# Performance work log

Measured on AMD Instinct MI355X. Metric: run time of the kernel, lower is better.

The kernel has to match this reference:

```python
import jax, jax.numpy as jnp
import numpy as np

DIM = 1024
NUM_HEADS = 16
HEAD_DIM = DIM // NUM_HEADS
SCALE = HEAD_DIM ** -0.5


def setup_inputs() -> dict:
    key = jax.random.key(0)
    ks = jax.random.split(key, 6)
    B, N, C = 2, 2048, DIM
    std = C ** -0.5
    return {
        "x_t": jax.random.normal(ks[0], (B, N, C), dtype=jnp.float32),
        "x_s": jax.random.normal(ks[1], (B, N, C), dtype=jnp.float32),
        "W_q": jax.random.normal(ks[2], (C, C), dtype=jnp.float32) * std,
        "W_kv": jax.random.normal(ks[3], (C, 2 * C), dtype=jnp.float32) * std,
        "W_fuse": jax.random.normal(ks[4], (C, C), dtype=jnp.float32) * std,
        "b_fuse": jax.random.normal(ks[5], (C,), dtype=jnp.float32) * 0.01,
    }


def reference(x_t, x_s, W_q, W_kv, W_fuse, b_fuse):
    B, N, C = x_t.shape
    H, D = NUM_HEADS, HEAD_DIM
    # q projection (no bias, qkv_bias=False): [B,N,C] -> [B,H,N,D]
    q = (x_t @ W_q).reshape(B, N, H, D).transpose(0, 2, 1, 3)
    # kv projection: [B,N,2C] -> k,v each [B,H,N,D]
    kv = (x_s @ W_kv).reshape(B, N, 2, H, D).transpose(2, 0, 3, 1, 4)
    k, v = kv[0], kv[1]
    # attention scores [B,H,N,N]
    attn = jnp.einsum("bhnd,bhmd->bhnm", q, k) * SCALE
    attn = jax.nn.softmax(attn, axis=-1)
    # weighted values -> [B,N,C]
    a = jnp.einsum("bhnm,bhmd->bhnd", attn, v).transpose(0, 2, 1, 3).reshape(B, N, C)
    # fuse projection (with bias); dropouts are identity (p=0)
    return a @ W_fuse + b_fuse
```

## Files before the change

### kernel.cpp

```cpp
#include <hip/hip_runtime.h>

#define SEQ 2048

typedef short short8 __attribute__((ext_vector_type(8)));
typedef float floatx4 __attribute__((ext_vector_type(4)));
typedef unsigned int uint2v __attribute__((ext_vector_type(2)));
typedef unsigned int uint4v __attribute__((ext_vector_type(4)));
typedef __fp16 f16x8 __attribute__((ext_vector_type(8)));

static __device__ __forceinline__ unsigned short f2bf(float f) {
    unsigned int u = __builtin_bit_cast(unsigned int, f);
    u = (u + 0x7fffu + ((u >> 16) & 1u)) >> 16;
    return (unsigned short)u;
}

#if __has_builtin(__builtin_amdgcn_cvt_pk_bf16_f32)
typedef __bf16 bf16x2 __attribute__((ext_vector_type(2)));
static __device__ __forceinline__ unsigned int pk_bf16(float a, float b) {
    bf16x2 v = __builtin_amdgcn_cvt_pk_bf16_f32(a, b);
    return __builtin_bit_cast(unsigned int, v);
}
#else
static __device__ __forceinline__ unsigned int pk_bf16(float a, float b) {
    return (unsigned int)f2bf(a) | ((unsigned int)f2bf(b) << 16);
}
#endif

static __device__ __forceinline__ unsigned int pk_f16(float a, float b) {
    auto v = __builtin_amdgcn_cvt_pkrtz(a, b);
    return __builtin_bit_cast(unsigned int, v);
}

#define GLD16(gp, lp)                                                        \
    __builtin_amdgcn_global_load_lds(                                        \
        (const __attribute__((address_space(1))) unsigned int*)(gp),         \
        (__attribute__((address_space(3))) unsigned int*)(lp), 16, 0, 0)

__global__ void cvt2_kernel(const float4* __restrict__ a, const float4* __restrict__ b,
                            ushort4* __restrict__ oa, ushort4* __restrict__ ob, float sa) {
    int i = blockIdx.x * blockDim.x + threadIdx.x;
    if (i < 1048576) {
        float4 v = a[i];
        ushort4 o;
        o.x = f2bf(v.x * sa); o.y = f2bf(v.y * sa);
        o.z = f2bf(v.z * sa); o.w = f2bf(v.w * sa);
        oa[i] = o;
    } else {
        int j = i - 1048576;
        float4 v = b[j];
        ushort4 o;
        o.x = f2bf(v.x); o.y = f2bf(v.y);
        o.z = f2bf(v.z); o.w = f2bf(v.w);
        ob[j] = o;
    }
}

__global__ void transpose_all(const float* __restrict__ Wq, const float* __restrict__ Wkv,
                              const float* __restrict__ Wf,
                              unsigned short* __restrict__ oq, unsigned short* __restrict__ okv,
                              unsigned short* __restrict__ of_) {
    __shared__ float tile[32][33];
    int bx = blockIdx.x;
    const float* in; unsigned short* out; int N, t;
    if (bx < 1024)      { in = Wq;  out = oq;  N = 1024; t = bx; }
    else if (bx < 3072) { in = Wkv; out = okv; N = 2048; t = bx - 1024; }
    else                { in = Wf;  out = of_; N = 1024; t = bx - 3072; }
    int nb = N >> 5;
    int n0 = (t % nb) * 32, k0 = (t / nb) * 32;
    int tx = threadIdx.x, ty = threadIdx.y;
#pragma unroll
    for (int i = 0; i < 4; i++)
        tile[ty + i * 8][tx] = in[(size_t)(k0 + ty + i * 8) * N + n0 + tx];
    __syncthreads();
#pragma unroll
    for (int i = 0; i < 4; i++)
        out[(size_t)(n0 + ty + i * 8) * 1024 + k0 + tx] = f2bf(tile[tx][ty + i * 8]);
}

__global__ __launch_bounds__(256, 3)
void gemm_qkv(const unsigned short* __restrict__ xt,
              const unsigned short* __restrict__ xs,
              const unsigned short* __restrict__ wq,
              const unsigned short* __restrict__ wkv,
              unsigned short* __restrict__ q_ws,
              unsigned short* __restrict__ k_ws,
              unsigned short* __restrict__ vt_ws) {
    __shared__ unsigned short sA[128][64];
    __shared__ unsigned short sB[128][64];
    int tid = threadIdx.x, wave = tid >> 6, lane = tid & 63;
    int l15 = lane & 15, quad = lane >> 4;
    int cx = blockIdx.x;
    bool isq = cx < 8;
    const unsigned short* A  = isq ? xt : xs;
    const unsigned short* Bt = isq ? wq : wkv;
    int C0 = (isq ? cx : cx - 8) * 128;
    int R0 = blockIdx.y * 128;
    int wr = (wave >> 1) * 64, wc = (wave & 1) * 64;
    int srow = lane >> 3, scol = (lane & 7) * 8;

    floatx4 acc[4][4];
#pragma unroll
    for (int i = 0; i < 4; i++)
#pragma unroll
        for (int j = 0; j < 4; j++) acc[i][j] = (floatx4){0.f, 0.f, 0.f, 0.f};

    for (int kt = 0; kt < 16; kt++) {
        __syncthreads();
#pragma unroll
        for (int c = 0; c < 4; c++) {
            int rb = wave * 32 + c * 8;
            GLD16(&A [(size_t)(R0 + rb + srow) * 1024 + kt * 64 + scol], &sA[rb][0]);
            GLD16(&Bt[(size_t)(C0 + rb + srow) * 1024 + kt * 64 + scol], &sB[rb][0]);
        }
        __syncthreads();
#pragma unroll
        for (int ks = 0; ks < 2; ks++) {
            short8 af[4], bf[4];
#pragma unroll
            for (int mt = 0; mt < 4; mt++)
                af[mt] = *(const short8*)&sA[wr + mt * 16 + l15][ks * 32 + quad * 8];
#pragma unroll
            for (int nt = 0; nt < 4; nt++)
                bf[nt] = *(const short8*)&sB[wc + nt * 16 + l15][ks * 32 + quad * 8];
#pragma unroll
            for (int mt = 0; mt < 4; mt++)
#pragma unroll
                for (int nt = 0; nt < 4; nt++)
                    acc[mt][nt] = __builtin_amdgcn_mfma_f32_16x16x32_bf16(af[mt], bf[nt], acc[mt][nt], 0, 0, 0);
        }
    }

    int b = R0 >> 11, nb0 = (R0 & 2047) + wr;
#pragma unroll
    for (int mt = 0; mt < 4; mt++) {
#pragma unroll
        for (int nt = 0; nt < 4; nt++) {
            int col = C0 + wc + nt * 16 + l15;
            if (isq) {
                int h = col >> 6, d = col & 63;
#pragma unroll
                for (int r = 0; r < 4; r++) {
                    int n = nb0 + mt * 16 + quad * 4 + r;
                    q_ws[((size_t)((b * 16 + h) * 2048 + n)) * 64 + d] = f2bf(acc[mt][nt][r]);
                }
            } else if (col < 1024) {
                int h = col >> 6, d = col & 63;
#pragma unroll
                for (int r = 0; r < 4; r++) {
                    int n = nb0 + mt * 16 + quad * 4 + r;
                    k_ws[((size_t)((b * 16 + h) * 2048 + n)) * 64 + (d ^ ((n & 7) << 3))] = f2bf(acc[mt][nt][r]);
                }
            } else {
                int cc = col - 1024, h = cc >> 6, d = cc & 63;
                int n = nb0 + mt * 16 + quad * 4;
                uint2v pk;
                pk.x = pk_f16(acc[mt][nt][0], acc[mt][nt][1]);
                pk.y = pk_f16(acc[mt][nt][2], acc[mt][nt][3]);
                *(uint2v*)&vt_ws[((size_t)((b * 16 + h) * 64 + d)) * 2048 + n] = pk;
            }
        }
    }
}

__global__ __launch_bounds__(256, 3)
void gemm_fuse(const unsigned short* __restrict__ A,
               const unsigned short* __restrict__ Bt,
               float* __restrict__ out, const float* __restrict__ bias) {
    __shared__ unsigned short sA[128][64];
    __shared__ unsigned short sB[64][64];
    int tid = threadIdx.x, wave = tid >> 6, lane = tid & 63;
    int l15 = lane & 15, quad = lane >> 4;
    int R0 = blockIdx.y * 128, C0 = blockIdx.x * 64;
    int wr = (wave >> 1) * 64, wc = (wave & 1) * 32;
    int srow = lane >> 3, scol = (lane & 7) * 8;

    floatx4 acc[4][2];
#pragma unroll
    for (int i = 0; i < 4; i++)
#pragma unroll
        for (int j = 0; j < 2; j++) acc[i][j] = (floatx4){0.f, 0.f, 0.f, 0.f};

    for (int kt = 0; kt < 16; kt++) {
        __syncthreads();
#pragma unroll
        for (int c = 0; c < 4; c++) {
            int rb = wave * 32 + c * 8;
            GLD16(&A[(size_t)(R0 + rb + srow) * 1024 + kt * 64 + scol], &sA[rb][0]);
        }
#pragma unroll
        for (int c = 0; c < 2; c++) {
            int rb = wave * 16 + c * 8;
            GLD16(&Bt[(size_t)(C0 + rb + srow) * 1024 + kt * 64 + scol], &sB[rb][0]);
        }
        __syncthreads();
#pragma unroll
        for (int ks = 0; ks < 2; ks++) {
            short8 af[4], bf[2];
#pragma unroll
            for (int mt = 0; mt < 4; mt++)
                af[mt] = *(const short8*)&sA[wr + mt * 16 + l15][ks * 32 + quad * 8];
#pragma unroll
            for (int nt = 0; nt < 2; nt++)
                bf[nt] = *(const short8*)&sB[wc + nt * 16 + l15][ks * 32 + quad * 8];
#pragma unroll
            for (int mt = 0; mt < 4; mt++)
#pragma unroll
                for (int nt = 0; nt < 2; nt++)
                    acc[mt][nt] = __builtin_amdgcn_mfma_f32_16x16x32_bf16(af[mt], bf[nt], acc[mt][nt], 0, 0, 0);
        }
    }

#pragma unroll
    for (int mt = 0; mt < 4; mt++) {
#pragma unroll
        for (int r = 0; r < 4; r++) {
            int row = R0 + wr + mt * 16 + quad * 4 + r;
#pragma unroll
            for (int nt = 0; nt < 2; nt++) {
                int col = C0 + wc + nt * 16 + l15;
                out[(size_t)row * 1024 + col] = acc[mt][nt][r] + bias[col];
            }
        }
    }
}

__global__ __launch_bounds__(256, 2)
void attn_kernel(const unsigned short* __restrict__ Q,
                 const unsigned short* __restrict__ K,
                 const unsigned short* __restrict__ Vt,
                 unsigned short* __restrict__ Aout) {
    __shared__ __align__(16) unsigned short smem[32768];
    __shared__ float lred[4][4][16];

    int tid = threadIdx.x, wave = tid >> 6, lane = tid & 63;
    int l15 = lane & 15, quad = lane >> 4;

    int id = blockIdx.x;
    int logical = (id & 7) * 128 + (id >> 3);
    int bh = logical >> 5, qt = logical & 31;
    int b = bh >> 4, h = bh & 15;
    int qr0 = qt * 64;

    const unsigned short* Qp = Q + (size_t)bh * SEQ * 64;
    const unsigned short* Kp = K + (size_t)bh * SEQ * 64;
    const unsigned short* Vp = Vt + (size_t)bh * 64 * SEQ;

    int wk0 = wave * 16;
    int WB = wave * 8192;

#define STAGE(t, s)                                                           \
    {                                                                         \
        _Pragma("unroll")                                                     \
        for (int j = 0; j < 2; j++)                                           \
            GLD16(&Kp[(size_t)((t) * 64 + wk0 + j * 8 + (lane >> 3)) * 64 +   \
                      (lane & 7) * 8],                                        \
                  &smem[WB + (s) * 2048 + j * 512]);                          \
        _Pragma("unroll")                                                     \
        for (int j = 0; j < 2; j++) {                                         \
            int dsrc = j * 32 + (lane >> 1);                                  \
            int hb = (((lane & 1) ^ ((dsrc >> 2) & 1)) << 3);                 \
            GLD16(&Vp[(size_t)dsrc * 2048 + (t) * 64 + wk0 + hb],             \
                  &smem[WB + (s) * 2048 + 1024 + j * 512]);                   \
        }                                                                     \
    }

    short8 qf[4][2];
#pragma unroll
    for (int nt = 0; nt < 4; nt++)
#pragma unroll
        for (int ks = 0; ks < 2; ks++)
            qf[nt][ks] = *(const short8*)&Qp[(size_t)(qr0 + nt * 16 + l15) * 64 + ks * 32 + quad * 8];

    STAGE(0, 0) STAGE(1, 1) STAGE(2, 2) STAGE(3, 3)

    floatx4 of[4][4];
#pragma unroll
    for (int i = 0; i < 4; i++)
#pragma unroll
        for (int j = 0; j < 4; j++) of[i][j] = (floatx4){0.f, 0.f, 0.f, 0.f};
    floatx4 of_l[4];
#pragma unroll
    for (int i = 0; i < 4; i++) of_l[i] = (floatx4){0.f, 0.f, 0.f, 0.f};

    f16x8 vones;
#pragma unroll
    for (int i = 0; i < 8; i++) vones[i] = (__fp16)1.0f;

    int ksw = (l15 & 7) << 3;
    int ka0 = l15 * 64 + ((quad * 8) ^ ksw);
    int ka1 = l15 * 64 + ((32 + quad * 8) ^ ksw);

    asm volatile("s_waitcnt vmcnt(0)" ::: "memory");

    auto compute_pair = [&](int sA, int sB) {
        int b0 = WB + sA * 2048, b1 = WB + sB * 2048;
        __builtin_amdgcn_s_setprio(1);
        uint2v pka[4], pkb[4];
        {
            short8 kf0 = *(const short8*)&smem[b0 + ka0];
            short8 kf1 = *(const short8*)&smem[b0 + ka1];
#pragma unroll
            for (int nt = 0; nt < 4; nt++) {
                floatx4 z = (floatx4){0.f, 0.f, 0.f, 0.f};
                floatx4 s = __builtin_amdgcn_mfma_f32_16x16x32_bf16(kf0, qf[nt][0], z, 0, 0, 0);
                s = __builtin_amdgcn_mfma_f32_16x16x32_bf16(kf1, qf[nt][1], s, 0, 0, 0);
                pka[nt].x = pk_f16(__builtin_amdgcn_exp2f(s[0]), __builtin_amdgcn_exp2f(s[1]));
                pka[nt].y = pk_f16(__builtin_amdgcn_exp2f(s[2]), __builtin_amdgcn_exp2f(s[3]));
            }
        }
        {
            short8 kf0 = *(const short8*)&smem[b1 + ka0];
            short8 kf1 = *(const short8*)&smem[b1 + ka1];
#pragma unroll
            for (int nt = 0; nt < 4; nt++) {
                floatx4 z = (floatx4){0.f, 0.f, 0.f, 0.f};
                floatx4 s = __builtin_amdgcn_mfma_f32_16x16x32_bf16(kf0, qf[nt][0], z, 0, 0, 0);
                s = __builtin_amdgcn_mfma_f32_16x16x32_bf16(kf1, qf[nt][1], s, 0, 0, 0);
                pkb[nt].x = pk_f16(__builtin_amdgcn_exp2f(s[0]), __builtin_amdgcn_exp2f(s[1]));
                pkb[nt].y = pk_f16(__builtin_amdgcn_exp2f(s[2]), __builtin_amdgcn_exp2f(s[3]));
            }
        }
#pragma unroll
        for (int dt = 0; dt < 4; dt++) {
            int d = dt * 16 + l15;
            int vo = d * 16 + ((quad * 4) ^ (((d >> 2) & 1) << 3));
            uint2v va = *(const uint2v*)&smem[b0 + 1024 + vo];
            uint2v vb = *(const uint2v*)&smem[b1 + 1024 + vo];
            f16x8 vf = __builtin_bit_cast(f16x8, (uint4v){va.x, va.y, vb.x, vb.y});
#pragma unroll
            for (int nt = 0; nt < 4; nt++) {
                f16x8 pf = __builtin_bit_cast(f16x8,
                    (uint4v){pka[nt].x, pka[nt].y, pkb[nt].x, pkb[nt].y});
                of[dt][nt] = __builtin_amdgcn_mfma_f32_16x16x32_f16(vf, pf, of[dt][nt], 0, 0, 0);
            }
        }
#pragma unroll
        for (int nt = 0; nt < 4; nt++) {
            f16x8 pf = __builtin_bit_cast(f16x8,
                (uint4v){pka[nt].x, pka[nt].y, pkb[nt].x, pkb[nt].y});
            of_l[nt] = __builtin_amdgcn_mfma_f32_16x16x32_f16(vones, pf, of_l[nt], 0, 0, 0);
        }
        __builtin_amdgcn_s_setprio(0);
    };

#pragma unroll 2
    for (int p = 0; p < 14; p++) {
        int sA = (p & 1) * 2;
        compute_pair(sA, sA + 1);
        STAGE(2 * p + 4, sA) STAGE(2 * p + 5, sA + 1)
        asm volatile("s_waitcnt vmcnt(8)" ::: "memory");
    }
    compute_pair(0, 1);
    asm volatile("s_waitcnt vmcnt(0)" ::: "memory");
    compute_pair(2, 3);
#undef STAGE

    if (quad == 0) {
#pragma unroll
        for (int nt = 0; nt < 4; nt++) lred[wave][nt][l15] = of_l[nt][0];
    }
    __syncthreads();

    float* red = (float*)smem;

#define RED_WRITE(C, DTC)                                                          \
    _Pragma("unroll")                                                              \
    for (int nt = 0; nt < 4; nt++)                                                 \
        *(floatx4*)&red[((C) * 4 + wave) * 1024 + nt * 256 + lane * 4] = of[DTC][nt];

#define RED_STORE(DT, C, W0, W1, W2)                                               \
    {                                                                              \
        size_t obase = (size_t)(b * SEQ + qr0) * 1024 + h * 64 + (DT) * 16 + quad * 4; \
        _Pragma("unroll")                                                          \
        for (int nt = 0; nt < 4; nt++) {                                           \
            floatx4 a0 = *(const floatx4*)&red[((C) * 4 + (W0)) * 1024 + nt * 256 + lane * 4]; \
            floatx4 a1 = *(const floatx4*)&red[((C) * 4 + (W1)) * 1024 + nt * 256 + lane * 4]; \
            floatx4 a2 = *(const floatx4*)&red[((C) * 4 + (W2)) * 1024 + nt * 256 + lane * 4]; \
            floatx4 s = of[DT][nt] + a0 + a1 + a2;                                 \
            float lt = lred[0][nt][l15] + lred[1][nt][l15] + lred[2][nt][l15] + lred[3][nt][l15]; \
            float inv = 1.f / lt;                                                  \
            uint2v o;                                                              \
            o.x = pk_bf16(s[0] * inv, s[1] * inv);                                 \
            o.y = pk_bf16(s[2] * inv, s[3] * inv);                                 \
            *(uint2v*)&Aout[obase + (size_t)(nt * 16 + l15) * 1024] = o;           \
        }                                                                          \
    }

    RED_WRITE(0, 0)
    RED_WRITE(1, 1)
    __syncthreads();
    if (wave == 0)      RED_STORE(0, 0, 1, 2, 3)
    else if (wave == 1) RED_STORE(1, 1, 0, 2, 3)
    __syncthreads();
    RED_WRITE(0, 2)
    RED_WRITE(1, 3)
    __syncthreads();
    if (wave == 2)      RED_STORE(2, 0, 0, 1, 3)
    else if (wave == 3) RED_STORE(3, 1, 0, 1, 2)
#undef RED_WRITE
#undef RED_STORE
}

extern "C" void kernel_launch(void* const* d_in, const int* in_sizes, int n_in,
                              void* d_out, int out_size, void* d_ws, size_t ws_size,
                              hipStream_t stream) {
    const float* x_t  = (const float*)d_in[0];
    const float* x_s  = (const float*)d_in[1];
    const float* W_q  = (const float*)d_in[2];
    const float* W_kv = (const float*)d_in[3];
    const float* W_f  = (const float*)d_in[4];
    const float* b_f  = (const float*)d_in[5];
    float* out = (float*)d_out;

    char* ws = (char*)d_ws;
    const size_t MB = 1u << 20;
    unsigned short* xt_bf = (unsigned short*)(ws);
    unsigned short* xs_bf = (unsigned short*)(ws + 8 * MB);
    unsigned short* wq_t  = (unsigned short*)(ws + 16 * MB);
    unsigned short* wkv_t = (unsigned short*)(ws + 18 * MB);
    unsigned short* wf_t  = (unsigned short*)(ws + 22 * MB);
    unsigned short* q_ws  = (unsigned short*)(ws + 24 * MB);
    unsigned short* k_ws  = (unsigned short*)(ws + 32 * MB);
    unsigned short* vt_ws = (unsigned short*)(ws + 40 * MB);
    unsigned short* a_ws  = (unsigned short*)(ws + 48 * MB);

    cvt2_kernel<<<8192, 256, 0, stream>>>((const float4*)x_t, (const float4*)x_s,
                                          (ushort4*)xt_bf, (ushort4*)xs_bf,
                                          0.125f * 1.44269504088896340736f);
    transpose_all<<<4096, dim3(32, 8), 0, stream>>>(W_q, W_kv, W_f, wq_t, wkv_t, wf_t);

    gemm_qkv<<<dim3(24, 32), 256, 0, stream>>>(xt_bf, xs_bf, wq_t, wkv_t, q_ws, k_ws, vt_ws);
    attn_kernel<<<1024, 256, 0, stream>>>(q_ws, k_ws, vt_ws, a_ws);
    gemm_fuse<<<dim3(16, 32), 256, 0, stream>>>(a_ws, wf_t, out, b_f);
}
```

Measured before the change: 205.3 us.

## Merge prep kernels, stage QKV epilogue via LDS, load V directly in attention

```diff
diff --git a/kernel.cpp b/kernel.cpp
--- a/kernel.cpp
+++ b/kernel.cpp
@@ -36,38 +36,40 @@
         (const __attribute__((address_space(1))) unsigned int*)(gp),         \
         (__attribute__((address_space(3))) unsigned int*)(lp), 16, 0, 0)
 
-__global__ void cvt2_kernel(const float4* __restrict__ a, const float4* __restrict__ b,
-                            ushort4* __restrict__ oa, ushort4* __restrict__ ob, float sa) {
-    int i = blockIdx.x * blockDim.x + threadIdx.x;
-    if (i < 1048576) {
-        float4 v = a[i];
-        ushort4 o;
-        o.x = f2bf(v.x * sa); o.y = f2bf(v.y * sa);
-        o.z = f2bf(v.z * sa); o.w = f2bf(v.w * sa);
-        oa[i] = o;
-    } else {
-        int j = i - 1048576;
-        float4 v = b[j];
-        ushort4 o;
-        o.x = f2bf(v.x); o.y = f2bf(v.y);
-        o.z = f2bf(v.z); o.w = f2bf(v.w);
-        ob[j] = o;
-    }
-}
-
-__global__ void transpose_all(const float* __restrict__ Wq, const float* __restrict__ Wkv,
-                              const float* __restrict__ Wf,
-                              unsigned short* __restrict__ oq, unsigned short* __restrict__ okv,
-                              unsigned short* __restrict__ of_) {
+__global__ void prep_kernel(const float4* __restrict__ xa, const float4* __restrict__ xb,
+                            ushort4* __restrict__ oa, ushort4* __restrict__ ob, float sa,
+                            const float* __restrict__ Wq, const float* __restrict__ Wkv,
+                            const float* __restrict__ Wf,
+                            unsigned short* __restrict__ oq, unsigned short* __restrict__ okv,
+                            unsigned short* __restrict__ of_) {
     __shared__ float tile[32][33];
-    int bx = blockIdx.x;
+    int bx = blockIdx.x, tid = threadIdx.x;
+    if (bx < 8192) {
+        int i = bx * 256 + tid;
+        if (i < 1048576) {
+            float4 v = xa[i];
+            ushort4 o;
+            o.x = f2bf(v.x * sa); o.y = f2bf(v.y * sa);
+            o.z = f2bf(v.z * sa); o.w = f2bf(v.w * sa);
+            oa[i] = o;
+        } else {
+            int j = i - 1048576;
+            float4 v = xb[j];
+            ushort4 o;
+            o.x = f2bf(v.x); o.y = f2bf(v.y);
+            o.z = f2bf(v.z); o.w = f2bf(v.w);
+            ob[j] = o;
+        }
+        return;
+    }
+    int t2 = bx - 8192;
     const float* in; unsigned short* out; int N, t;
-    if (bx < 1024)      { in = Wq;  out = oq;  N = 1024; t = bx; }
-    else if (bx < 3072) { in = Wkv; out = okv; N = 2048; t = bx - 1024; }
-    else                { in = Wf;  out = of_; N = 1024; t = bx - 3072; }
+    if (t2 < 1024)      { in = Wq;  out = oq;  N = 1024; t = t2; }
+    else if (t2 < 3072) { in = Wkv; out = okv; N = 2048; t = t2 - 1024; }
+    else                { in = Wf;  out = of_; N = 1024; t = t2 - 3072; }
     int nb = N >> 5;
     int n0 = (t % nb) * 32, k0 = (t / nb) * 32;
-    int tx = threadIdx.x, ty = threadIdx.y;
+    int tx = tid & 31, ty = tid >> 5;
 #pragma unroll
     for (int i = 0; i < 4; i++)
         tile[ty + i * 8][tx] = in[(size_t)(k0 + ty + i * 8) * N + n0 + tx];
@@ -85,12 +87,13 @@
               unsigned short* __restrict__ q_ws,
               unsigned short* __restrict__ k_ws,
               unsigned short* __restrict__ vt_ws) {
-    __shared__ unsigned short sA[128][64];
-    __shared__ unsigned short sB[128][64];
+    __shared__ __align__(16) unsigned short smem_[16384];
+    auto sA = (unsigned short(*)[64])smem_;
+    auto sB = (unsigned short(*)[64])(smem_ + 8192);
     int tid = threadIdx.x, wave = tid >> 6, lane = tid & 63;
     int l15 = lane & 15, quad = lane >> 4;
     int cx = blockIdx.x;
-    bool isq = cx < 8;
+    bool isq = cx < 8, isv = cx >= 16;
     const unsigned short* A  = isq ? xt : xs;
     const unsigned short* Bt = isq ? wq : wkv;
     int C0 = (isq ? cx : cx - 8) * 128;
@@ -130,34 +133,55 @@
         }
     }
 
-    int b = R0 >> 11, nb0 = (R0 & 2047) + wr;
-#pragma unroll
-    for (int mt = 0; mt < 4; mt++) {
-#pragma unroll
-        for (int nt = 0; nt < 4; nt++) {
-            int col = C0 + wc + nt * 16 + l15;
-            if (isq) {
-                int h = col >> 6, d = col & 63;
-#pragma unroll
-                for (int r = 0; r < 4; r++) {
-                    int n = nb0 + mt * 16 + quad * 4 + r;
-                    q_ws[((size_t)((b * 16 + h) * 2048 + n)) * 64 + d] = f2bf(acc[mt][nt][r]);
-                }
-            } else if (col < 1024) {
-                int h = col >> 6, d = col & 63;
-#pragma unroll
-                for (int r = 0; r < 4; r++) {
-                    int n = nb0 + mt * 16 + quad * 4 + r;
-                    k_ws[((size_t)((b * 16 + h) * 2048 + n)) * 64 + (d ^ ((n & 7) << 3))] = f2bf(acc[mt][nt][r]);
-                }
-            } else {
-                int cc = col - 1024, h = cc >> 6, d = cc & 63;
-                int n = nb0 + mt * 16 + quad * 4;
+    int b = R0 >> 11, n0 = R0 & 2047;
+    __syncthreads();
+
+    if (!isv) {
+#pragma unroll
+        for (int mt = 0; mt < 4; mt++)
+#pragma unroll
+            for (int nt = 0; nt < 4; nt++) {
+                int col = wc + nt * 16 + l15;
+#pragma unroll
+                for (int r = 0; r < 4; r++)
+                    smem_[(wr + mt * 16 + quad * 4 + r) * 128 + col] = f2bf(acc[mt][nt][r]);
+            }
+        __syncthreads();
+        unsigned short* out = isq ? q_ws : k_ws;
+#pragma unroll
+        for (int i = 0; i < 8; i++) {
+            int u = tid + i * 256;
+            int row = u >> 4, colg = u & 15;
+            int n = n0 + row;
+            int gc = C0 + colg * 8;
+            int h = gc >> 6, d0 = gc & 63;
+            int dd = isq ? d0 : ((((d0 >> 3) ^ (n & 7)) << 3));
+            *(uint4v*)&out[((size_t)((b * 16 + h) * 2048 + n)) * 64 + dd] =
+                *(const uint4v*)&smem_[row * 128 + colg * 8];
+        }
+    } else {
+#pragma unroll
+        for (int mt = 0; mt < 4; mt++)
+#pragma unroll
+            for (int nt = 0; nt < 4; nt++) {
+                int cc = wc + nt * 16 + l15;
+                int nl4 = (wr + mt * 16 + quad * 4) >> 2;
+                int sw = nl4 ^ ((cc & 3) << 1);
                 uint2v pk;
                 pk.x = pk_f16(acc[mt][nt][0], acc[mt][nt][1]);
                 pk.y = pk_f16(acc[mt][nt][2], acc[mt][nt][3]);
-                *(uint2v*)&vt_ws[((size_t)((b * 16 + h) * 64 + d)) * 2048 + n] = pk;
-            }
+                *(uint2v*)&smem_[cc * 128 + (sw << 2)] = pk;
+            }
+        __syncthreads();
+        int cb = C0 - 1024;
+#pragma unroll
+        for (int i = 0; i < 8; i++) {
+            int u = tid + i * 256;
+            int cc = u >> 4, ng = u & 15;
+            int sw0 = (2 * ng) ^ ((cc & 3) << 1);
+            uint4v val = *(const uint4v*)&smem_[cc * 128 + (sw0 << 2)];
+            int ccv = cb + cc, h = ccv >> 6, d = ccv & 63;
+            *(uint4v*)&vt_ws[((size_t)((b * 16 + h) * 64 + d)) * 2048 + n0 + ng * 8] = val;
         }
     }
 }
@@ -224,12 +248,12 @@
     }
 }
 
-__global__ __launch_bounds__(256, 2)
+__global__ __launch_bounds__(256, 3)
 void attn_kernel(const unsigned short* __restrict__ Q,
                  const unsigned short* __restrict__ K,
                  const unsigned short* __restrict__ Vt,
                  unsigned short* __restrict__ Aout) {
-    __shared__ __align__(16) unsigned short smem[32768];
+    __shared__ __align__(16) unsigned short smem[16384];
     __shared__ float lred[4][4][16];
 
     int tid = threadIdx.x, wave = tid >> 6, lane = tid & 63;
@@ -246,23 +270,18 @@
     const unsigned short* Vp = Vt + (size_t)bh * 64 * SEQ;
 
     int wk0 = wave * 16;
-    int WB = wave * 8192;
-
-#define STAGE(t, s)                                                           \
+    int WB = wave * 4096;
+
+#define STAGEK(t)                                                             \
     {                                                                         \
         _Pragma("unroll")                                                     \
         for (int j = 0; j < 2; j++)                                           \
             GLD16(&Kp[(size_t)((t) * 64 + wk0 + j * 8 + (lane >> 3)) * 64 +   \
                       (lane & 7) * 8],                                        \
-                  &smem[WB + (s) * 2048 + j * 512]);                          \
-        _Pragma("unroll")                                                     \
-        for (int j = 0; j < 2; j++) {                                         \
-            int dsrc = j * 32 + (lane >> 1);                                  \
-            int hb = (((lane & 1) ^ ((dsrc >> 2) & 1)) << 3);                 \
-            GLD16(&Vp[(size_t)dsrc * 2048 + (t) * 64 + wk0 + hb],             \
-                  &smem[WB + (s) * 2048 + 1024 + j * 512]);                   \
-        }                                                                     \
-    }
+                  &smem[WB + ((t) & 3) * 1024 + j * 512]);                    \
+    }
+
+    STAGEK(0) STAGEK(1) STAGEK(2) STAGEK(3)
 
     short8 qf[4][2];
 #pragma unroll
@@ -270,8 +289,6 @@
 #pragma unroll
         for (int ks = 0; ks < 2; ks++)
             qf[nt][ks] = *(const short8*)&Qp[(size_t)(qr0 + nt * 16 + l15) * 64 + ks * 32 + quad * 8];
-
-    STAGE(0, 0) STAGE(1, 1) STAGE(2, 2) STAGE(3, 3)
 
     floatx4 of[4][4];
 #pragma unroll
@@ -290,10 +307,16 @@
     int ka0 = l15 * 64 + ((quad * 8) ^ ksw);
     int ka1 = l15 * 64 + ((32 + quad * 8) ^ ksw);
 
-    asm volatile("s_waitcnt vmcnt(0)" ::: "memory");
-
-    auto compute_pair = [&](int sA, int sB) {
-        int b0 = WB + sA * 2048, b1 = WB + sB * 2048;
+    auto compute_pair = [&](int p) {
+        int b0 = WB + ((2 * p) & 3) * 1024, b1 = b0 + 1024;
+        int t0 = 2 * p * 64, t1 = t0 + 64;
+        uint2v va[4], vb[4];
+#pragma unroll
+        for (int dt = 0; dt < 4; dt++) {
+            const unsigned short* vr = &Vp[(size_t)(dt * 16 + l15) * 2048 + wk0 + quad * 4];
+            va[dt] = *(const uint2v*)&vr[t0];
+            vb[dt] = *(const uint2v*)&vr[t1];
+        }
         __builtin_amdgcn_s_setprio(1);
         uint2v pka[4], pkb[4];
         {
@@ -322,11 +345,8 @@
         }
 #pragma unroll
         for (int dt = 0; dt < 4; dt++) {
-            int d = dt * 16 + l15;
-            int vo = d * 16 + ((quad * 4) ^ (((d >> 2) & 1) << 3));
-            uint2v va = *(const uint2v*)&smem[b0 + 1024 + vo];
-            uint2v vb = *(const uint2v*)&smem[b1 + 1024 + vo];
-            f16x8 vf = __builtin_bit_cast(f16x8, (uint4v){va.x, va.y, vb.x, vb.y});
+            f16x8 vf = __builtin_bit_cast(f16x8,
+                (uint4v){va[dt].x, va[dt].y, vb[dt].x, vb[dt].y});
 #pragma unroll
             for (int nt = 0; nt < 4; nt++) {
                 f16x8 pf = __builtin_bit_cast(f16x8,
@@ -343,17 +363,28 @@
         __builtin_amdgcn_s_setprio(0);
     };
 
-#pragma unroll 2
-    for (int p = 0; p < 14; p++) {
-        int sA = (p & 1) * 2;
-        compute_pair(sA, sA + 1);
-        STAGE(2 * p + 4, sA) STAGE(2 * p + 5, sA + 1)
-        asm volatile("s_waitcnt vmcnt(8)" ::: "memory");
-    }
-    compute_pair(0, 1);
+    asm volatile("s_waitcnt vmcnt(12)" ::: "memory");
+    compute_pair(0);
+    __builtin_amdgcn_sched_barrier(0);
+    STAGEK(4) STAGEK(5)
+    __builtin_amdgcn_sched_barrier(0);
+    asm volatile("s_waitcnt vmcnt(12)" ::: "memory");
+    compute_pair(1);
+    __builtin_amdgcn_sched_barrier(0);
+    STAGEK(6) STAGEK(7)
+    __builtin_amdgcn_sched_barrier(0);
+    for (int p = 2; p < 14; p++) {
+        asm volatile("s_waitcnt vmcnt(4)" ::: "memory");
+        compute_pair(p);
+        __builtin_amdgcn_sched_barrier(0);
+        STAGEK(2 * p + 4) STAGEK(2 * p + 5)
+        __builtin_amdgcn_sched_barrier(0);
+    }
+    asm volatile("s_waitcnt vmcnt(4)" ::: "memory");
+    compute_pair(14);
     asm volatile("s_waitcnt vmcnt(0)" ::: "memory");
-    compute_pair(2, 3);
-#undef STAGE
+    compute_pair(15);
+#undef STAGEK
 
     if (quad == 0) {
 #pragma unroll
@@ -424,10 +455,10 @@
     unsigned short* vt_ws = (unsigned short*)(ws + 40 * MB);
     unsigned short* a_ws  = (unsigned short*)(ws + 48 * MB);
 
-    cvt2_kernel<<<8192, 256, 0, stream>>>((const float4*)x_t, (const float4*)x_s,
-                                          (ushort4*)xt_bf, (ushort4*)xs_bf,
-                                          0.125f * 1.44269504088896340736f);
-    transpose_all<<<4096, dim3(32, 8), 0, stream>>>(W_q, W_kv, W_f, wq_t, wkv_t, wf_t);
+    prep_kernel<<<12288, 256, 0, stream>>>((const float4*)x_t, (const float4*)x_s,
+                                           (ushort4*)xt_bf, (ushort4*)xs_bf,
+                                           0.125f * 1.44269504088896340736f,
+                                           W_q, W_kv, W_f, wq_t, wkv_t, wf_t);
 
     gemm_qkv<<<dim3(24, 32), 256, 0, stream>>>(xt_bf, xs_bf, wq_t, wkv_t, q_ws, k_ws, vt_ws);
     attn_kernel<<<1024, 256, 0, stream>>>(q_ws, k_ws, vt_ws, a_ws);
```

Result: slower. 232.6 us (+13.3%).
